# Optimization experiments

Measured on AMD Instinct MI355X. Metric: run time of the kernel, lower is better.

Reference implementation:

```python
import jax, jax.numpy as jnp
import numpy as np
import math

QUERY_DIM = 128
SCALE = 1.0 / math.sqrt(QUERY_DIM)

def setup_inputs() -> dict:
    key = jax.random.key(0)
    k1, k2, k3 = jax.random.split(key, 3)
    B, Q, K, D = 16, 2048, 2048, 128
    return {
        "query": jax.random.normal(k1, (B, Q, D), dtype=jnp.float32),
        "keys": jax.random.normal(k2, (B, K, D), dtype=jnp.float32),
        "values": jax.random.normal(k3, (B, K, D), dtype=jnp.float32),
    }

def reference(query, keys, values):
    # energy[b,q,k] = sum_d query[b,q,d] * keys[b,k,d], scaled then softmax over k
    energy = jnp.einsum("bqd,bkd->bqk", query, keys) * SCALE
    attn = jax.nn.softmax(energy, axis=2)
    # linear combination over values
    return jnp.einsum("bqk,bkv->bqv", attn, values)
```

## Files before the change

### kernel.cpp

```cpp
#include <hip/hip_runtime.h>
#include <hip/hip_bf16.h>


#define BATCH 16
#define QLEN 2048
#define KLEN 2048
#define DIM 128
#define BM 64
#define BN 64
#define NT (KLEN / BN)

#define VBYTES 16384
#define SMEM_BYTES 34048

typedef __attribute__((ext_vector_type(8))) short bf16x8;
typedef __attribute__((ext_vector_type(4))) float f32x4;

__device__ __forceinline__ short f2bf(float x) {
    union { float f; unsigned u; } v; v.f = x;
    unsigned r = v.u + 0x7FFFu + ((v.u >> 16) & 1u);
    return (short)(r >> 16);
}
__device__ __forceinline__ unsigned pkbf(float a, float b) {
    union { float f; unsigned u; } x, y; x.f = a; y.f = b;
    unsigned ra = x.u + 0x7FFFu + ((x.u >> 16) & 1u);
    unsigned rb = y.u + 0x7FFFu + ((y.u >> 16) & 1u);
    return __builtin_amdgcn_perm(rb, ra, 0x07060302u);
}
__device__ __forceinline__ float fexp2(float x) {
#if __has_builtin(__builtin_amdgcn_exp2f)
    return __builtin_amdgcn_exp2f(x);
#else
    return exp2f(x);
#endif
}

#define GLOAD_LDS16(g, l) \
    __builtin_amdgcn_global_load_lds((__attribute__((address_space(1))) void*)(g), \
                                     (__attribute__((address_space(3))) void*)(l), 16, 0, 0)

#define TSTR 72
__global__ __launch_bounds__(256) void prepass_kernel(
    const float* __restrict__ kg, const float* __restrict__ vg,
    unsigned short* __restrict__ Kws, unsigned short* __restrict__ Vtws)
{
    __shared__ unsigned short T[DIM * TSTR];
    const int tid = threadIdx.x;
    const int kb  = blockIdx.x * BN;
    const int b   = blockIdx.y;
    const float* kt = kg + ((size_t)b * KLEN + kb) * DIM;
    const float* vt = vg + ((size_t)b * KLEN + kb) * DIM;

    unsigned short* koF = Kws + ((size_t)b * KLEN + kb) * DIM;
#pragma unroll
    for (int j = 0; j < 4; ++j) {
        int c = tid + 256 * j;
        int key   = c & 63;
        int chunk = c >> 6;
        float4 k0 = *(const float4*)(kt + key * DIM + chunk * 8);
        float4 k1 = *(const float4*)(kt + key * DIM + chunk * 8 + 4);
        uint4 w;
        w.x = pkbf(k0.x, k0.y); w.y = pkbf(k0.z, k0.w);
        w.z = pkbf(k1.x, k1.y); w.w = pkbf(k1.z, k1.w);
        int r    = (key & 3) | ((key & 8) >> 1) | ((key & 16) >> 1)
                 | ((key & 4) << 2) | (key & 32);
        int kw_  = r >> 5;
        int half = (r >> 4) & 1;
        int lm_  = r & 15;
        int dk   = chunk >> 2;
        int qd   = chunk & 3;
        int soff = (((kw_ * 4 + dk) * 2 + half) * 4 + qd) * 128 + lm_ * 8;
        *(uint4*)(koF + soff) = w;
    }

#pragma unroll
    for (int j = 0; j < 8; ++j) {
        int idx = tid + 256 * j;
        int key = idx >> 5;
        int d4  = (idx & 31) * 4;
        float4 vv = *(const float4*)(vt + key * DIM + d4);
        T[(d4 + 0) * TSTR + key] = (unsigned short)f2bf(vv.x);
        T[(d4 + 1) * TSTR + key] = (unsigned short)f2bf(vv.y);
        T[(d4 + 2) * TSTR + key] = (unsigned short)f2bf(vv.z);
        T[(d4 + 3) * TSTR + key] = (unsigned short)f2bf(vv.w);
    }
    __syncthreads();
    unsigned short* vo = Vtws + (size_t)b * DIM * KLEN + kb;
#pragma unroll
    for (int j = 0; j < 4; ++j) {
        int c = tid + 256 * j;
        int d = c >> 3;
        int g = c & 7;
        uint4 u = *(const uint4*)&T[d * TSTR + g * 8];
        *(uint4*)(vo + (size_t)d * KLEN + g * 8) = u;
    }
}

__global__ __launch_bounds__(256, 2) void attn_flash_kernel(
    const float* __restrict__ qg,
    const unsigned short* __restrict__ Kws,
    const unsigned short* __restrict__ Vtws,
    float* __restrict__ outg)
{
    __shared__ __align__(16) char SMC[SMEM_BYTES];

    const int tid  = threadIdx.x;
    const int wave = tid >> 6;
    const int lane = tid & 63;
    const int lm   = lane & 15;
    const int quad = lane >> 4;
    const int rw   = wave >> 1;
    const int kw   = wave & 1;

    const int n  = blockIdx.y * gridDim.x + blockIdx.x;
    const int np = (n & 7) * 64 + (n >> 3);
    const int b     = np >> 5;
    const int qbase = (np & 31) * BM + rw * 32;

    const float QSCALE = 0.08838834764831845f * 1.4426950408889634f;

    bf16x8 qfA[4], qfB[4];
    {
        const float* qrowA = qg + (size_t)(b * QLEN + qbase + lm) * DIM;
        const float* qrowB = qrowA + 16 * DIM;
#pragma unroll
        for (int dk = 0; dk < 4; ++dk) {
            int d0 = dk * 32 + quad * 8;
            float4 a = *(const float4*)(qrowA + d0);
            float4 c = *(const float4*)(qrowA + d0 + 4);
            uint4 u;
            u.x = pkbf(a.x*QSCALE, a.y*QSCALE); u.y = pkbf(a.z*QSCALE, a.w*QSCALE);
            u.z = pkbf(c.x*QSCALE, c.y*QSCALE); u.w = pkbf(c.z*QSCALE, c.w*QSCALE);
            qfA[dk] = *(bf16x8*)&u;
            float4 e = *(const float4*)(qrowB + d0);
            float4 g = *(const float4*)(qrowB + d0 + 4);
            uint4 v;
            v.x = pkbf(e.x*QSCALE, e.y*QSCALE); v.y = pkbf(e.z*QSCALE, e.w*QSCALE);
            v.z = pkbf(g.x*QSCALE, g.y*QSCALE); v.w = pkbf(g.z*QSCALE, g.w*QSCALE);
            qfB[dk] = *(bf16x8*)&v;
        }
    }

    f32x4 OA[8], OB[8];
#pragma unroll
    for (int i = 0; i < 8; ++i) { OA[i] = 0.0f; OB[i] = 0.0f; }
    float lrA = 0.f, lrB = 0.f;

    const unsigned short* kfp = Kws + (size_t)b * KLEN * DIM
                              + kw * 4096 + lane * 8;

    const unsigned short* Vtb = Vtws + (size_t)b * DIM * KLEN;
    const char* vdma[4];
    {
        int gv  = lane & 7;
        int d0v = wave * 32 + (lane >> 3);
#pragma unroll
        for (int i = 0; i < 4; ++i) {
            int dv = d0v + 8 * i;
            vdma[i] = (const char*)Vtb + (size_t)dv * (KLEN * 2) + ((gv ^ (dv & 7)) << 4);
        }
    }

    const int vfo = lm * 128 + (((kw * 4 + quad) ^ (lm & 7)) << 4);

    auto dma = [&](int tt, int bb) {
        char* ldsV = SMC + bb * VBYTES + wave * 4096;
        size_t vo = (size_t)tt * 128;
#pragma unroll
        for (int i = 0; i < 4; ++i)
            GLOAD_LDS16(vdma[i] + vo, ldsV + i * 1024);
    };

    f32x4 SP0a, SP1a, SP0b, SP1b;
    bf16x8 vp[8];
    bf16x8 kp[8];

#pragma unroll
    for (int i = 0; i < 8; ++i) kp[i] = *(const bf16x8*)(kfp + i * 512);
    dma(0, 0);
    __syncthreads();
    {
        dma(1, 1);
        f32x4 S0a = 0.0f, S1a = 0.0f, S0b = 0.0f, S1b = 0.0f;
#pragma unroll
        for (int dk = 0; dk < 4; ++dk) {
            S0a = __builtin_amdgcn_mfma_f32_16x16x32_bf16(kp[2*dk],   qfA[dk], S0a, 0, 0, 0);
            S0b = __builtin_amdgcn_mfma_f32_16x16x32_bf16(kp[2*dk],   qfB[dk], S0b, 0, 0, 0);
            S1a = __builtin_amdgcn_mfma_f32_16x16x32_bf16(kp[2*dk+1], qfA[dk], S1a, 0, 0, 0);
            S1b = __builtin_amdgcn_mfma_f32_16x16x32_bf16(kp[2*dk+1], qfB[dk], S1b, 0, 0, 0);
        }
        const char* bufV = SMC;
#pragma unroll
        for (int dt = 0; dt < 8; ++dt)
            vp[dt] = *(const bf16x8*)(bufV + vfo + dt * 2048);
#pragma unroll
        for (int i = 0; i < 8; ++i)
            kp[i] = *(const bf16x8*)(kfp + 8192 + i * 512);
        SP0a = S0a; SP1a = S1a; SP0b = S0b; SP1b = S1b;
    }
    __syncthreads();

    for (int t = 1; t < NT; ++t) {
        if (t + 1 < NT) dma(t + 1, (t + 1) & 1);

        float a0 = fexp2(SP0a[0]), a1 = fexp2(SP0a[1]), a2 = fexp2(SP0a[2]), a3 = fexp2(SP0a[3]);
        float a4 = fexp2(SP1a[0]), a5 = fexp2(SP1a[1]), a6 = fexp2(SP1a[2]), a7 = fexp2(SP1a[3]);
        float b0 = fexp2(SP0b[0]), b1 = fexp2(SP0b[1]), b2 = fexp2(SP0b[2]), b3 = fexp2(SP0b[3]);
        float b4 = fexp2(SP1b[0]), b5 = fexp2(SP1b[1]), b6 = fexp2(SP1b[2]), b7 = fexp2(SP1b[3]);
        uint4 puA, puB;
        puA.x = pkbf(a0,a1); puA.y = pkbf(a2,a3); puA.z = pkbf(a4,a5); puA.w = pkbf(a6,a7);
        puB.x = pkbf(b0,b1); puB.y = pkbf(b2,b3); puB.z = pkbf(b4,b5); puB.w = pkbf(b6,b7);
        bf16x8 pfA = *(bf16x8*)&puA;
        bf16x8 pfB = *(bf16x8*)&puB;
        lrA += ((a0+a1)+(a2+a3)) + ((a4+a5)+(a6+a7));
        lrB += ((b0+b1)+(b2+b3)) + ((b4+b5)+(b6+b7));

        f32x4 S0a = 0.0f, S1a = 0.0f, S0b = 0.0f, S1b = 0.0f;
#pragma unroll
        for (int dk = 0; dk < 4; ++dk) {
            S0a = __builtin_amdgcn_mfma_f32_16x16x32_bf16(kp[2*dk],   qfA[dk], S0a, 0, 0, 0);
            S0b = __builtin_amdgcn_mfma_f32_16x16x32_bf16(kp[2*dk],   qfB[dk], S0b, 0, 0, 0);
            S1a = __builtin_amdgcn_mfma_f32_16x16x32_bf16(kp[2*dk+1], qfA[dk], S1a, 0, 0, 0);
            S1b = __builtin_amdgcn_mfma_f32_16x16x32_bf16(kp[2*dk+1], qfB[dk], S1b, 0, 0, 0);
        }

        if (t + 1 < NT) {
            const unsigned short* kt1 = kfp + (size_t)(t + 1) * 8192;
#pragma unroll
            for (int i = 0; i < 8; ++i)
                kp[i] = *(const bf16x8*)(kt1 + i * 512);
        }

#pragma unroll
        for (int dt = 0; dt < 8; ++dt) {
            OA[dt] = __builtin_amdgcn_mfma_f32_16x16x32_bf16(vp[dt], pfA, OA[dt], 0, 0, 0);
            OB[dt] = __builtin_amdgcn_mfma_f32_16x16x32_bf16(vp[dt], pfB, OB[dt], 0, 0, 0);
        }

        {
            const char* bufV = SMC + (t & 1) * VBYTES;
#pragma unroll
            for (int dt = 0; dt < 8; ++dt)
                vp[dt] = *(const bf16x8*)(bufV + vfo + dt * 2048);
        }

        SP0a = S0a; SP1a = S1a; SP0b = S0b; SP1b = S1b;

        __syncthreads();
    }

    {
        float a0 = fexp2(SP0a[0]), a1 = fexp2(SP0a[1]), a2 = fexp2(SP0a[2]), a3 = fexp2(SP0a[3]);
        float a4 = fexp2(SP1a[0]), a5 = fexp2(SP1a[1]), a6 = fexp2(SP1a[2]), a7 = fexp2(SP1a[3]);
        float b0 = fexp2(SP0b[0]), b1 = fexp2(SP0b[1]), b2 = fexp2(SP0b[2]), b3 = fexp2(SP0b[3]);
        float b4 = fexp2(SP1b[0]), b5 = fexp2(SP1b[1]), b6 = fexp2(SP1b[2]), b7 = fexp2(SP1b[3]);
        uint4 puA, puB;
        puA.x = pkbf(a0,a1); puA.y = pkbf(a2,a3); puA.z = pkbf(a4,a5); puA.w = pkbf(a6,a7);
        puB.x = pkbf(b0,b1); puB.y = pkbf(b2,b3); puB.z = pkbf(b4,b5); puB.w = pkbf(b6,b7);
        bf16x8 pfA = *(bf16x8*)&puA;
        bf16x8 pfB = *(bf16x8*)&puB;
        lrA += ((a0+a1)+(a2+a3)) + ((a4+a5)+(a6+a7));
        lrB += ((b0+b1)+(b2+b3)) + ((b4+b5)+(b6+b7));
#pragma unroll
        for (int dt = 0; dt < 8; ++dt) {
            OA[dt] = __builtin_amdgcn_mfma_f32_16x16x32_bf16(vp[dt], pfA, OA[dt], 0, 0, 0);
            OB[dt] = __builtin_amdgcn_mfma_f32_16x16x32_bf16(vp[dt], pfB, OB[dt], 0, 0, 0);
        }
    }

    lrA += __shfl_xor(lrA, 16, 64); lrA += __shfl_xor(lrA, 32, 64);
    lrB += __shfl_xor(lrB, 16, 64); lrB += __shfl_xor(lrB, 32, 64);

    float* Orw = (float*)SMC + rw * 4288;
    if (kw == 1) {
#pragma unroll
        for (int dt = 0; dt < 8; ++dt) {
            *(f32x4*)&Orw[lm*132        + dt*16 + quad*4] = OA[dt];
            *(f32x4*)&Orw[(16+lm)*132   + dt*16 + quad*4] = OB[dt];
        }
        if (lane < 16)      Orw[4224 + lm]      = lrA;
        else if (lane < 32) Orw[4224 + 16 + lm] = lrB;
    }
    __syncthreads();
    if (kw == 0) {
        float invA = 1.0f / (lrA + Orw[4224 + lm]);
        float invB = 1.0f / (lrB + Orw[4224 + 16 + lm]);
        float* orowA = outg + (size_t)(b * QLEN + qbase + lm) * DIM;
        float* orowB = orowA + 16 * DIM;
#pragma unroll
        for (int dt = 0; dt < 8; ++dt) {
            f32x4 oA = *(const f32x4*)&Orw[lm*132      + dt*16 + quad*4];
            f32x4 oB = *(const f32x4*)&Orw[(16+lm)*132 + dt*16 + quad*4];
            *(f32x4*)&orowA[dt*16 + quad*4] = (OA[dt] + oA) * invA;
            *(f32x4*)&orowB[dt*16 + quad*4] = (OB[dt] + oB) * invB;
        }
    }
}

extern "C" void kernel_launch(void* const* d_in, const int* in_sizes, int n_in,
                              void* d_out, int out_size, void* d_ws, size_t ws_size,
                              hipStream_t stream) {
    const float* q = (const float*)d_in[0];
    const float* k = (const float*)d_in[1];
    const float* v = (const float*)d_in[2];
    float* o = (float*)d_out;
    unsigned short* Kws  = (unsigned short*)d_ws;
    unsigned short* Vtws = Kws + (size_t)BATCH * KLEN * DIM;
    dim3 grid(KLEN / BN, BATCH);
    prepass_kernel<<<grid, 256, 0, stream>>>(k, v, Kws, Vtws);
    dim3 grid2(QLEN / BM, BATCH);
    attn_flash_kernel<<<grid2, 256, 0, stream>>>(q, Kws, Vtws, o);
}
```

Before: 130.6 us.

## Load V fragments directly from global in MFMA order, dropping LDS staging

The prepass now writes V in a fragment-swizzled layout that matches the per-lane MFMA operand order, the same way K is already stored. The attention kernel then loads V fragments straight from global memory into registers instead of using async global-to-LDS DMA into a double buffer. This removes the LDS round trip and the per-tile __syncthreads. In exchange, each wave issues its own global loads for V, so blocks that share a batch no longer share V through LDS and load latency is exposed to register-level prefetch only.

```diff
diff --git a/kernel.cpp b/kernel.cpp
--- a/kernel.cpp
+++ b/kernel.cpp
@@ -10,7 +10,6 @@
 #define BN 64
 #define NT (KLEN / BN)
 
-#define VBYTES 16384
 #define SMEM_BYTES 34048
 
 typedef __attribute__((ext_vector_type(8))) short bf16x8;
@@ -34,10 +33,6 @@
     return exp2f(x);
 #endif
 }
-
-#define GLOAD_LDS16(g, l) \
-    __builtin_amdgcn_global_load_lds((__attribute__((address_space(1))) void*)(g), \
-                                     (__attribute__((address_space(3))) void*)(l), 16, 0, 0)
 
 #define TSTR 72
 __global__ __launch_bounds__(256) void prepass_kernel(
@@ -85,14 +80,19 @@
         T[(d4 + 3) * TSTR + key] = (unsigned short)f2bf(vv.w);
     }
     __syncthreads();
-    unsigned short* vo = Vtws + (size_t)b * DIM * KLEN + kb;
+    unsigned short* voF = Vtws + ((size_t)b * KLEN + kb) * DIM;
 #pragma unroll
     for (int j = 0; j < 4; ++j) {
         int c = tid + 256 * j;
         int d = c >> 3;
         int g = c & 7;
         uint4 u = *(const uint4*)&T[d * TSTR + g * 8];
-        *(uint4*)(vo + (size_t)d * KLEN + g * 8) = u;
+        int kw_  = g >> 2;
+        int qd   = g & 3;
+        int dt   = d >> 4;
+        int lm_  = d & 15;
+        int soff = ((kw_ * 8 + dt) * 4 + qd) * 128 + lm_ * 8;
+        *(uint4*)(voF + soff) = u;
     }
 }
 
@@ -148,28 +148,8 @@
 
     const unsigned short* kfp = Kws + (size_t)b * KLEN * DIM
                               + kw * 4096 + lane * 8;
-
-    const unsigned short* Vtb = Vtws + (size_t)b * DIM * KLEN;
-    const char* vdma[4];
-    {
-        int gv  = lane & 7;
-        int d0v = wave * 32 + (lane >> 3);
-#pragma unroll
-        for (int i = 0; i < 4; ++i) {
-            int dv = d0v + 8 * i;
-            vdma[i] = (const char*)Vtb + (size_t)dv * (KLEN * 2) + ((gv ^ (dv & 7)) << 4);
-        }
-    }
-
-    const int vfo = lm * 128 + (((kw * 4 + quad) ^ (lm & 7)) << 4);
-
-    auto dma = [&](int tt, int bb) {
-        char* ldsV = SMC + bb * VBYTES + wave * 4096;
-        size_t vo = (size_t)tt * 128;
-#pragma unroll
-        for (int i = 0; i < 4; ++i)
-            GLOAD_LDS16(vdma[i] + vo, ldsV + i * 1024);
-    };
+    const unsigned short* vfp = Vtws + (size_t)b * KLEN * DIM
+                              + kw * 4096 + lane * 8;
 
     f32x4 SP0a, SP1a, SP0b, SP1b;
     bf16x8 vp[8];
@@ -177,10 +157,9 @@
 
 #pragma unroll
     for (int i = 0; i < 8; ++i) kp[i] = *(const bf16x8*)(kfp + i * 512);
-    dma(0, 0);
-    __syncthreads();
+#pragma unroll
+    for (int i = 0; i < 8; ++i) vp[i] = *(const bf16x8*)(vfp + i * 512);
     {
-        dma(1, 1);
         f32x4 S0a = 0.0f, S1a = 0.0f, S0b = 0.0f, S1b = 0.0f;
 #pragma unroll
         for (int dk = 0; dk < 4; ++dk) {
@@ -189,20 +168,13 @@
             S1a = __builtin_amdgcn_mfma_f32_16x16x32_bf16(kp[2*dk+1], qfA[dk], S1a, 0, 0, 0);
             S1b = __builtin_amdgcn_mfma_f32_16x16x32_bf16(kp[2*dk+1], qfB[dk], S1b, 0, 0, 0);
         }
-        const char* bufV = SMC;
-#pragma unroll
-        for (int dt = 0; dt < 8; ++dt)
-            vp[dt] = *(const bf16x8*)(bufV + vfo + dt * 2048);
 #pragma unroll
         for (int i = 0; i < 8; ++i)
             kp[i] = *(const bf16x8*)(kfp + 8192 + i * 512);
         SP0a = S0a; SP1a = S1a; SP0b = S0b; SP1b = S1b;
     }
-    __syncthreads();
 
     for (int t = 1; t < NT; ++t) {
-        if (t + 1 < NT) dma(t + 1, (t + 1) & 1);
-
         float a0 = fexp2(SP0a[0]), a1 = fexp2(SP0a[1]), a2 = fexp2(SP0a[2]), a3 = fexp2(SP0a[3]);
         float a4 = fexp2(SP1a[0]), a5 = fexp2(SP1a[1]), a6 = fexp2(SP1a[2]), a7 = fexp2(SP1a[3]);
         float b0 = fexp2(SP0b[0]), b1 = fexp2(SP0b[1]), b2 = fexp2(SP0b[2]), b3 = fexp2(SP0b[3]);
@@ -238,15 +210,13 @@
         }
 
         {
-            const char* bufV = SMC + (t & 1) * VBYTES;
+            const unsigned short* vt1 = vfp + (size_t)t * 8192;
 #pragma unroll
             for (int dt = 0; dt < 8; ++dt)
-                vp[dt] = *(const bf16x8*)(bufV + vfo + dt * 2048);
+                vp[dt] = *(const bf16x8*)(vt1 + dt * 512);
         }
 
         SP0a = S0a; SP1a = S1a; SP0b = S0b; SP1b = S1b;
-
-        __syncthreads();
     }
 
     {
```

Result: slower. 136.5 us (+4.5%).
